# Kernel tuning notes

Measured on AMD Instinct MI355X. Metric: run time of the kernel, lower is better.

## Reference

```python
import jax, jax.numpy as jnp
import numpy as np

B = 128
IN = 256
NLVL = 6
KLVL = 3
CH = 4
C = 4 * CH * CH          # 64 channels per node
OU = 8                   # out_filter_siz_u
OV = 8                   # out_filter_siz_v
NK = 2 ** KLVL           # 8 leaf nodes per axis
W_SCALE = 1.0 / 16.0     # ~1/sqrt(2*2*C) so 7 stacked relu-convs stay numerically sane


def setup_inputs() -> dict:
    key = jax.random.key(0)
    ks = jax.random.split(key, 2 * NLVL + 4)
    fx = IN // 2 ** NLVL  # 4: input patch filter size
    inp = {}
    inp["in_data"] = jax.random.normal(ks[0], (B, IN, IN, 1), jnp.float32)
    inp["in_filter"] = jax.random.normal(ks[1], (fx, fx, 1, C), jnp.float32) * W_SCALE
    inp["in_bias"] = jnp.zeros((C,), jnp.float32)
    i = 2
    for lvl in range(1, NLVL + 1):
        n = 2 ** min(lvl, KLVL)  # node grid: grows to 2^klvl then stays
        inp[f"f{lvl}"] = jax.random.normal(ks[i], (n, n, 2, 2, C, C), jnp.float32) * W_SCALE
        inp[f"b{lvl}"] = jnp.zeros((n, n, C), jnp.float32)
        i += 1
    inp["Wd"] = jax.random.normal(ks[i], (NK, NK, 2, C, OU * OV), jnp.float32) * W_SCALE
    return inp


def _node_conv(x, w, b):
    # x: [Nu,Nv,B,H,W,C]; w: [Nu,Nv,2,2,C,C]; 2x2 stride-2 VALID conv per node
    Nu, Nv, Bn, H, W, Cc = x.shape
    xr = x.reshape(Nu, Nv, Bn, H // 2, 2, W // 2, 2, Cc)
    y = jnp.einsum('uvbhxwyc,uvxyco->uvbhwo', xr, w)
    return jax.nn.relu(y + b[:, :, None, None, None, :])


def _forward(in_data, in_filter, in_bias, fs, bs, Wd):
    Bn = in_data.shape[0]
    fx, fy = in_filter.shape[0], in_filter.shape[1]
    # input interp conv: stride == kernel -> non-overlapping patch GEMM
    xr = in_data[..., 0].reshape(Bn, in_data.shape[1] // fx, fx, in_data.shape[2] // fy, fy)
    x = jax.nn.relu(jnp.einsum('bxpyq,pqc->bxyc', xr, in_filter[:, :, 0, :]) + in_bias)
    x = x[None, None]  # [1,1,B,2^nlvl,2^nlvl,C] node grid
    for lvl in range(1, NLVL + 1):
        if lvl <= KLVL:
            # children (itu,itv) read parent (itu//2, itv//2)
            x = jnp.repeat(jnp.repeat(x, 2, axis=0), 2, axis=1)
        x = _node_conv(x, fs[lvl - 1], bs[lvl - 1])
    feats = x[:, :, :, 0, 0, :]  # [NK,NK,B,C]; spatial is 1x1 at level nlvl
    out = jnp.einsum('uvbc,uvrck->uvbrk', feats, Wd)  # r in {real, imag}
    out = out.reshape(NK, NK, Bn, 2, OU, OV)
    out = jnp.transpose(out, (2, 0, 4, 1, 5, 3))  # [B,itu,ou,itv,ov,2]
    return out.reshape(Bn, NK * OU, NK * OV, 2)


def reference(in_data, in_filter, in_bias, f1, b1, f2, b2, f3, b3, f4, b4, f5, b5, f6, b6, Wd):
    fs = (f1, f2, f3, f4, f5, f6)
    bs = (b1, b2, b3, b4, b5, b6)
    return _forward(in_data, in_filter, in_bias, fs, bs, Wd)
```

## Files before the change

### kernel.cpp

```cpp
#include <hip/hip_runtime.h>
#include <hip/hip_bf16.h>
#include <cstdint>
#include <cstddef>


typedef __attribute__((ext_vector_type(8))) short short8;
typedef __attribute__((ext_vector_type(4))) float f32x4;
typedef unsigned short ushort_t;

static __device__ __forceinline__ float b2f(const __hip_bfloat16 x) {
    return __bfloat162float(x);
}
static __device__ __forceinline__ ushort_t f2bf(float x) {
    __hip_bfloat16 h = __float2bfloat16(x);
    ushort_t u;
    __builtin_memcpy(&u, &h, 2);
    return u;
}
static __device__ __forceinline__ void gl_lds16(const void* g, void* l) {
    __builtin_amdgcn_global_load_lds(
        (const __attribute__((address_space(1))) void*)g,
        (__attribute__((address_space(3))) void*)l, 16, 0, 0);
}
#define WAIT_LGKM0() __builtin_amdgcn_s_waitcnt(0xC07F)
#define WAIT_VM0()   __builtin_amdgcn_s_waitcnt(0x0F70)

#define PREP_BLOCKS 2533

static __device__ __forceinline__ void prep_work(
    int gid, int isbf,
    const void* f1, const void* f2, const void* f3,
    const void* f4, const void* f5, const void* f6, const void* wdsrc,
    const void* b1, const void* b2, const void* b3,
    const void* b4, const void* b5, const void* b6,
    ushort_t* __restrict__ wbuf, ushort_t* __restrict__ wdbuf,
    float* __restrict__ bbuf)
{
    if (gid >= 648448) return;
    if (gid >= 630784) {
        const int bg = gid - 630784;
        const void* src; int base;
        if      (bg <   256) { src = b1; base = 0;     }
        else if (bg <  1280) { src = b2; base = 256;   }
        else if (bg <  5376) { src = b3; base = 1280;  }
        else if (bg <  9472) { src = b4; base = 5376;  }
        else if (bg < 13568) { src = b5; base = 9472;  }
        else                 { src = b6; base = 13568; }
        const int local = bg - base;
        bbuf[bg] = isbf ? b2f(((const __hip_bfloat16*)src)[local])
                        : ((const float*)src)[local];
        return;
    }
    if (gid >= 565248) {
        const int local = gid - 565248;
        const int lane = local & 63;
        const int slot = (local >> 6) & 15;
        const int site = local >> 10;
        const int ks2 = slot >> 3, nh = slot & 7, q = lane >> 4;
        const int n = nh * 16 + (lane & 15);
        const int r = n >> 6, kk = n & 63;
        const int cbase = ks2 * 32 + q * 8;
        ushort_t pk[8];
        if (isbf) {
            const ushort_t* s = (const ushort_t*)wdsrc;
            #pragma unroll
            for (int j = 0; j < 8; j++)
                pk[j] = s[(((size_t)(site * 2 + r) * 64 + cbase + j) * 64) + kk];
        } else {
            const float* s = (const float*)wdsrc;
            #pragma unroll
            for (int j = 0; j < 8; j++)
                pk[j] = f2bf(s[(((size_t)(site * 2 + r) * 64 + cbase + j) * 64) + kk]);
        }
        *(uint4*)&wdbuf[(size_t)local * 8] = *(uint4*)pk;
        return;
    }
    const void* fsrc; int base;
    if      (gid <   8192) { fsrc = f1; base = 0;      }
    else if (gid <  40960) { fsrc = f2; base = 8192;   }
    else if (gid < 172032) { fsrc = f3; base = 40960;  }
    else if (gid < 303104) { fsrc = f4; base = 172032; }
    else if (gid < 434176) { fsrc = f5; base = 303104; }
    else                   { fsrc = f6; base = 434176; }
    const int local = gid - base;
    const int lane = local & 63;
    const int slot = (local >> 6) & 7;
    const int sitetap = local >> 9;
    const int ks = slot >> 2, nh = slot & 3, q = lane >> 4;
    const int n = (lane & 15) + nh * 16;
    const int kbase = ks * 32 + q * 8;
    ushort_t pk[8];
    if (isbf) {
        const ushort_t* s = (const ushort_t*)fsrc + (size_t)sitetap * 4096;
        #pragma unroll
        for (int j = 0; j < 8; j++) pk[j] = s[(kbase + j) * 64 + n];
    } else {
        const float* s = (const float*)fsrc + (size_t)sitetap * 4096;
        #pragma unroll
        for (int j = 0; j < 8; j++) pk[j] = f2bf(s[(kbase + j) * 64 + n]);
    }
    *(uint4*)&wbuf[(size_t)gid * 8] = *(uint4*)pk;
}

static __device__ __forceinline__ void stage0_body(
    int blk, int isbf,
    const void* __restrict__ in_data, const void* __restrict__ filt,
    const void* __restrict__ bias, __hip_bfloat16* __restrict__ x0,
    int b_off, int Bc)
{
    const int X  = blk & 63;
    const int bl = blk >> 6;
    const int bg = bl + b_off;

    __shared__ float sIn[4][256];
    __shared__ float sF[16][64];
    __shared__ float sB[64];

    const int t = threadIdx.x;
    const size_t srow = ((size_t)bg * 256 + (size_t)X * 4) * 256;

    if (isbf) {
        const __hip_bfloat16* src = (const __hip_bfloat16*)in_data + srow;
        #pragma unroll
        for (int i = 0; i < 4; i++) {
            int flat = i * 256 + t;
            int p = flat >> 8, col = flat & 255;
            sIn[p][col] = b2f(src[(size_t)p * 256 + col]);
        }
        const __hip_bfloat16* fsrc = (const __hip_bfloat16*)filt;
        #pragma unroll
        for (int i = 0; i < 4; i++) {
            int flat = i * 256 + t;
            sF[flat >> 6][flat & 63] = b2f(fsrc[flat]);
        }
        if (t < 64) sB[t] = b2f(((const __hip_bfloat16*)bias)[t]);
    } else {
        const float* src = (const float*)in_data + srow;
        const int p = t >> 6, c4 = (t & 63) * 4;
        *(float4*)&sIn[p][c4] = *(const float4*)(src + (size_t)p * 256 + c4);
        const float* fsrc = (const float*)filt;
        #pragma unroll
        for (int i = 0; i < 4; i++) {
            int flat = i * 256 + t;
            sF[flat >> 6][flat & 63] = fsrc[flat];
        }
        if (t < 64) sB[t] = ((const float*)bias)[t];
    }
    __syncthreads();

    const int ty = t >> 4;
    const int tc = t & 15;

    float acc[4][4];
    {
        const float4 bv = *(const float4*)&sB[tc * 4];
        #pragma unroll
        for (int yi = 0; yi < 4; yi++) {
            acc[yi][0] = bv.x; acc[yi][1] = bv.y;
            acc[yi][2] = bv.z; acc[yi][3] = bv.w;
        }
    }

    #pragma unroll
    for (int p = 0; p < 4; p++) {
        float4 rin[4], rf[4];
        #pragma unroll
        for (int yi = 0; yi < 4; yi++)
            rin[yi] = *(const float4*)&sIn[p][ty * 16 + yi * 4];
        #pragma unroll
        for (int q = 0; q < 4; q++)
            rf[q] = *(const float4*)&sF[p * 4 + q][tc * 4];
        #pragma unroll
        for (int yi = 0; yi < 4; yi++) {
            #pragma unroll
            for (int q = 0; q < 4; q++) {
                const float a = ((const float*)&rin[yi])[q];
                acc[yi][0] = fmaf(a, rf[q].x, acc[yi][0]);
                acc[yi][1] = fmaf(a, rf[q].y, acc[yi][1]);
                acc[yi][2] = fmaf(a, rf[q].z, acc[yi][2]);
                acc[yi][3] = fmaf(a, rf[q].w, acc[yi][3]);
            }
        }
    }

    ushort_t* dst = (ushort_t*)x0;
    #pragma unroll
    for (int yi = 0; yi < 4; yi++) {
        uint2 pk;
        pk.x = (uint32_t)f2bf(fmaxf(acc[yi][0], 0.f))
             | ((uint32_t)f2bf(fmaxf(acc[yi][1], 0.f)) << 16);
        pk.y = (uint32_t)f2bf(fmaxf(acc[yi][2], 0.f))
             | ((uint32_t)f2bf(fmaxf(acc[yi][3], 0.f)) << 16);
        const int wpos = ty * 4 + yi;
        *(uint2*)(dst + ((size_t)(X * 64 + wpos) * Bc + bl) * 64 + tc * 4) = pk;
    }
}

__global__ __launch_bounds__(256) void k_prep0(
    const void* __restrict__ in_data,
    const void* f1, const void* f2, const void* f3,
    const void* f4, const void* f5, const void* f6, const void* wdsrc,
    const void* b1, const void* b2, const void* b3,
    const void* b4, const void* b5, const void* b6,
    ushort_t* __restrict__ wbuf, ushort_t* __restrict__ wdbuf,
    float* __restrict__ bbuf, int* __restrict__ flag,
    const void* __restrict__ filt, const void* __restrict__ bias0,
    __hip_bfloat16* __restrict__ x0, int Bc)
{
    __shared__ int sflag;
    const int t = threadIdx.x;
    if (t < 64) {
        const float v = __uint_as_float(((const uint32_t*)in_data)[t]);
        const bool plaus = (v == 0.0f) || (fabsf(v) > 1e-8f && fabsf(v) < 1e4f);
        const unsigned long long m = __ballot(plaus);
        if (t == 0) sflag = (__popcll(m) >= 48) ? 0 : 1;
    }
    __syncthreads();
    const int isbf = sflag;

    if (blockIdx.x < PREP_BLOCKS) {
        if (blockIdx.x == 0 && t == 0) *flag = isbf;
        prep_work(blockIdx.x * 256 + t, isbf,
                  f1, f2, f3, f4, f5, f6, wdsrc,
                  b1, b2, b3, b4, b5, b6, wbuf, wdbuf, bbuf);
    } else {
        stage0_body(blockIdx.x - PREP_BLOCKS, isbf, in_data, filt, bias0, x0, 0, Bc);
    }
}

__global__ __launch_bounds__(256) void k_stage0(
    const void* __restrict__ in_data, const void* __restrict__ filt,
    const void* __restrict__ bias, __hip_bfloat16* __restrict__ x0,
    const int* __restrict__ flag, int b_off, int Bc)
{
    stage0_body(blockIdx.x, *flag, in_data, filt, bias, x0, b_off, Bc);
}

__global__ __launch_bounds__(256, 2) void k_fused12(
    const __hip_bfloat16* __restrict__ xin,
    const ushort_t* __restrict__ w1,
    const ushort_t* __restrict__ w2,
    const float* __restrict__ b1, const float* __restrict__ b2,
    __hip_bfloat16* __restrict__ xout,
    int Bc, int mtiles)
{
    __shared__ __align__(16) ushort_t smem[27136];

    int idx = blockIdx.x;
    const int mt = idx % mtiles; idx /= mtiles;
    const int parent = idx & 3; idx >>= 2;
    const int wstrip = idx & 3;
    const int h2p = idx >> 2;
    const int ip = parent >> 1, jp = parent & 1;

    const int t = threadIdx.x;
    const int wave = t >> 6, lane = t & 63;
    const int lm = lane & 15, lq = lane >> 4;

    const size_t pstride = (size_t)Bc * 64;

    int brow = mt * 16 + lm;
    if (brow >= Bc) brow = Bc - 1;

    const ushort_t* w1site = w1 + (size_t)parent * 16384 + lane * 8;
    short8 breg[32];
    #pragma unroll
    for (int s = 0; s < 32; s++) breg[s] = *(const short8*)(w1site + s * 512);

    float bv1[4];
    #pragma unroll
    for (int fn = 0; fn < 4; fn++) bv1[fn] = b1[parent * 64 + fn * 16 + lm];

    const f32x4 zero = {0.f, 0.f, 0.f, 0.f};
    ushort_t* l1b = smem;
    const int wa = wave >> 1, wb = wave & 1;

    for (int pos = 0; pos < 4; pos++) {
        const int w2p = wstrip * 4 + pos;
        f32x4 acc[4];
        #pragma unroll
        for (int fn = 0; fn < 4; fn++) acc[fn] = zero;

        #pragma unroll
        for (int cd = 0; cd < 4; cd++) {
            const int hi0 = 4 * h2p + 2 * wa + (cd >> 1);
            const int wi0 = 4 * w2p + 2 * wb + (cd & 1);
            const __hip_bfloat16* ap =
                xin + ((size_t)hi0 * 64 + wi0) * pstride
                    + (size_t)brow * 64 + lq * 8;
            #pragma unroll
            for (int ks = 0; ks < 2; ks++) {
                short8 afr = *(const short8*)(ap + ks * 32);
                #pragma unroll
                for (int fn = 0; fn < 4; fn++)
                    acc[fn] = __builtin_amdgcn_mfma_f32_16x16x32_bf16(
                        afr, breg[cd * 8 + ks * 4 + fn], acc[fn], 0, 0, 0);
            }
        }
        ushort_t* dst = l1b + (pos * 4 + wave) * 1152;
        #pragma unroll
        for (int fn = 0; fn < 4; fn++) {
            #pragma unroll
            for (int r = 0; r < 4; r++) {
                const int m = lq * 4 + r;
                dst[m * 72 + fn * 16 + lm] =
                    f2bf(fmaxf(acc[fn][r] + bv1[fn], 0.f));
            }
        }
    }
    __syncthreads();

    {
        const int di = wave >> 1, dj = wave & 1;
        const int s2 = (2 * ip + di) * 4 + (2 * jp + dj);
        const ushort_t* w2site = w2 + (size_t)s2 * 16384 + lane * 8;
        short8 wreg[32];
        #pragma unroll
        for (int s = 0; s < 32; s++) wreg[s] = *(const short8*)(w2site + s * 512);

        float bv2[4];
        #pragma unroll
        for (int fn = 0; fn < 4; fn++) bv2[fn] = b2[s2 * 64 + fn * 16 + lm];

        ushort_t* so_buf = smem + 18432 + wave * 2176;

        for (int pos = 0; pos < 4; pos++) {
            const int w2p = wstrip * 4 + pos;
            f32x4 acc[4];
            #pragma unroll
            for (int fn = 0; fn < 4; fn++) acc[fn] = zero;

            #pragma unroll
            for (int ab = 0; ab < 4; ab++) {
                const ushort_t* sl = l1b + (pos * 4 + ab) * 1152;
                #pragma unroll
                for (int ks = 0; ks < 2; ks++) {
                    short8 afr = *(const short8*)&sl[lm * 72 + ks * 32 + lq * 8];
                    #pragma unroll
                    for (int fn = 0; fn < 4; fn++)
                        acc[fn] = __builtin_amdgcn_mfma_f32_16x16x32_bf16(
                            afr, wreg[ab * 8 + ks * 4 + fn], acc[fn], 0, 0, 0);
                }
            }

            #pragma unroll
            for (int fn = 0; fn < 4; fn++) {
                #pragma unroll
                for (int r = 0; r < 4; r++) {
                    const int m = lq * 4 + r;
                    so_buf[m * 68 + fn * 16 + lm] =
                        f2bf(fmaxf(acc[fn][r] + bv2[fn], 0.f));
                }
            }
            const size_t obase = ((size_t)s2 * 256 + h2p * 16 + w2p) * pstride;
            #pragma unroll
            for (int i2 = 0; i2 < 2; i2++) {
                const int task = i2 * 64 + lane;
                const int oct = task & 7, row = task >> 3;
                const int brw = mt * 16 + row;
                if (brw < Bc) {
                    *(uint4*)(xout + obase + (size_t)brw * 64 + oct * 8) =
                        *(const uint4*)&so_buf[row * 68 + oct * 8];
                }
            }
        }
    }
}

__global__ __launch_bounds__(256, 2) void k_level4(
    const __hip_bfloat16* __restrict__ xin,
    const ushort_t* __restrict__ wbuf,
    const float* __restrict__ bbuf,
    __hip_bfloat16* __restrict__ xout,
    int Nv_out, int HW, int Bc, int mtiles)
{
    __shared__ __align__(16) ushort_t smem[17408];

    int idx = blockIdx.x;
    const int mt = idx % mtiles; idx /= mtiles;
    const int w  = idx % HW; idx /= HW;
    const int h  = idx % HW; idx /= HW;
    const int Nv_in = Nv_out >> 1;
    const int vp = idx % Nv_in;
    const int up = idx / Nv_in;

    const int t = threadIdx.x;
    const int wave = t >> 6, lane = t & 63;
    const int lm = lane & 15, lq = lane >> 4;

    const int so = (2 * up + (wave >> 1)) * Nv_out + (2 * vp + (wave & 1));
    const int H_in = HW * 2;
    const size_t pstride = (size_t)Bc * 64;
    const size_t siteb = (size_t)(up * Nv_in + vp) * H_in * H_in * pstride;
    const ushort_t* wsite = wbuf + (size_t)so * 4 * 4096 + lane * 8;

    {
        const int hi = 2 * h + (wave >> 1), wi = 2 * w + (wave & 1);
        const size_t tapoff = siteb + ((size_t)hi * H_in + wi) * pstride;
        #pragma unroll
        for (int j = 0; j < 8; j++) {
            const int ks = j >> 2, mh = j & 3;
            int b = mt * 64 + mh * 16 + lm;
            if (b >= Bc) b = Bc - 1;
            gl_lds16(xin + tapoff + (size_t)b * 64 + ks * 32 + lq * 8,
                     &smem[(wave * 8 + j) * 512]);
        }
    }

    short8 breg[32];
    #pragma unroll
    for (int s = 0; s < 32; s++)
        breg[s] = *(const short8*)(wsite + s * 512);
    __builtin_amdgcn_sched_barrier(0);

    float bv[4];
    #pragma unroll
    for (int fn = 0; fn < 4; fn++) bv[fn] = bbuf[so * 64 + fn * 16 + lm];

    __syncthreads();

    const f32x4 zero = {0.f, 0.f, 0.f, 0.f};
    f32x4 acc[4][4];
    #pragma unroll
    for (int i = 0; i < 4; i++)
        #pragma unroll
        for (int j = 0; j < 4; j++) acc[i][j] = zero;

    #pragma unroll
    for (int tap = 0; tap < 4; tap++) {
        #pragma unroll
        for (int ks = 0; ks < 2; ks++) {
            #pragma unroll
            for (int fm = 0; fm < 4; fm++) {
                short8 a = *(const short8*)&smem[(tap * 8 + ks * 4 + fm) * 512 + lane * 8];
                #pragma unroll
                for (int fn = 0; fn < 4; fn++)
                    acc[fm][fn] = __builtin_amdgcn_mfma_f32_16x16x32_bf16(
                        a, breg[tap * 8 + ks * 4 + fn], acc[fm][fn], 0, 0, 0);
            }
        }
    }
    __syncthreads();

    ushort_t* so_buf = smem + wave * 4352;
    #pragma unroll
    for (int fm = 0; fm < 4; fm++) {
        #pragma unroll
        for (int fn = 0; fn < 4; fn++) {
            #pragma unroll
            for (int r = 0; r < 4; r++) {
                const int row = fm * 16 + lq * 4 + r;
                so_buf[row * 68 + fn * 16 + lm] =
                    f2bf(fmaxf(acc[fm][fn][r] + bv[fn], 0.f));
            }
        }
    }
    __syncthreads();

    const size_t obase = ((size_t)so * HW * HW + (size_t)h * HW + w) * pstride;
    #pragma unroll
    for (int i = 0; i < 8; i++) {
        const int task = i * 64 + lane;
        const int oct = task & 7, row = task >> 3;
        const int b = mt * 64 + row;
        if (b < Bc) {
            *(uint4*)(xout + obase + (size_t)b * 64 + oct * 8) =
                *(const uint4*)&so_buf[row * 68 + oct * 8];
        }
    }
}

__global__ __launch_bounds__(256) void k_f456(
    const __hip_bfloat16* __restrict__ xin,
    const ushort_t* __restrict__ w4, const ushort_t* __restrict__ w5,
    const ushort_t* __restrict__ w6, const ushort_t* __restrict__ wd,
    const float* __restrict__ b4, const float* __restrict__ b5,
    const float* __restrict__ b6,
    void* __restrict__ out, const int* __restrict__ flag,
    int Bc, int b_off, int mtiles)
{
    const int isbf = *flag;
    const int bx = blockIdx.x;
    const int mt = bx % mtiles;
    const int site = bx / mtiles;
    const int u = site >> 3, v = site & 7;

    __shared__ __align__(16) ushort_t smem[37376];

    const int t = threadIdx.x;
    const int wv = t >> 6, lane = t & 63;
    const int lm = lane & 15, lq = lane >> 4;

    const ushort_t* w6s = w6 + (size_t)site * 16384 + lane * 8;
    const ushort_t* wds = wd + (size_t)site * 8192  + lane * 8;

    float bv4[4], bv5[4];
    #pragma unroll
    for (int fn = 0; fn < 4; fn++) {
        bv4[fn] = b4[site * 64 + fn * 16 + lm];
        bv5[fn] = b5[site * 64 + fn * 16 + lm];
    }
    const float bv6 = b6[site * 64 + wv * 16 + lm];

    {
        const ushort_t* w4s = w4 + (size_t)site * 16384;
        #pragma unroll
        for (int s2 = 0; s2 < 8; s2++) {
            const int s = wv * 8 + s2;
            gl_lds16(w4s + s * 512 + lane * 8, &smem[s * 512]);
        }
    }
    __syncthreads();

    const f32x4 zero = {0.f, 0.f, 0.f, 0.f};
    const int h5 = wv >> 1, w5p = wv & 1;
    ushort_t* mid1w = smem + 16384 + wv * 4224;
    ushort_t* Aw = smem + 33280 + wv * 1024;
    const size_t pstride = (size_t)Bc * 64;

    int brow = mt * 16 + lm;
    if (brow >= Bc) brow = Bc - 1;
    const __hip_bfloat16* xbase =
        xin + (size_t)site * 64 * pstride + (size_t)brow * 64 + lq * 8;

    for (int i = 0; i < 4; i++) {
        const int h4 = 2 * h5 + (i >> 1), w4p = 2 * w5p + (i & 1);
        f32x4 acc[4];
        #pragma unroll
        for (int b_ = 0; b_ < 4; b_++) acc[b_] = zero;

        for (int tap = 0; tap < 4; tap++) {
            const int h3 = 2 * h4 + (tap >> 1), w3 = 2 * w4p + (tap & 1);
            const size_t poff = (size_t)(h3 * 8 + w3) * pstride;
            WAIT_LGKM0();
            #pragma unroll
            for (int ks = 0; ks < 2; ks++) {
                gl_lds16(xbase + poff + ks * 32, &Aw[ks * 512]);
            }
            WAIT_VM0();
            __builtin_amdgcn_sched_barrier(0);
            #pragma unroll
            for (int ks = 0; ks < 2; ks++) {
                short8 a = *(const short8*)&Aw[ks * 512 + lane * 8];
                #pragma unroll
                for (int fn = 0; fn < 4; fn++) {
                    short8 bfr = *(const short8*)&smem[(tap * 8 + ks * 4 + fn) * 512 + lane * 8];
                    acc[fn] = __builtin_amdgcn_mfma_f32_16x16x32_bf16(a, bfr, acc[fn], 0, 0, 0);
                }
            }
        }
        #pragma unroll
        for (int fn = 0; fn < 4; fn++) {
            #pragma unroll
            for (int r = 0; r < 4; r++) {
                const int m = lq * 4 + r;
                const int ch = fn * 16 + lm;
                mid1w[m * 264 + i * 64 + ch] =
                    f2bf(fmaxf(acc[fn][r] + bv4[fn], 0.f));
            }
        }
    }
    __syncthreads();

    {
        const ushort_t* w5s = w5 + (size_t)site * 16384;
        #pragma unroll
        for (int s2 = 0; s2 < 8; s2++) {
            const int s = wv * 8 + s2;
            gl_lds16(w5s + s * 512 + lane * 8, &smem[s * 512]);
        }
    }
    __syncthreads();

    short8 b3r[8];
    short8 wdr[4];
    {
        f32x4 acc2[4];
        #pragma unroll
        for (int b_ = 0; b_ < 4; b_++) acc2[b_] = zero;

        #pragma unroll
        for (int i = 0; i < 4; i++) {
            #pragma unroll
            for (int ks = 0; ks < 2; ks++) {
                short8 a0 = *(const short8*)&mid1w[lm * 264 + i * 64 + ks * 32 + lq * 8];
                #pragma unroll
                for (int fn = 0; fn < 4; fn++) {
                    short8 bfr = *(const short8*)&smem[(i * 8 + ks * 4 + fn) * 512 + lane * 8];
                    acc2[fn] = __builtin_amdgcn_mfma_f32_16x16x32_bf16(a0, bfr, acc2[fn], 0, 0, 0);
                }
            }
        }

        #pragma unroll
        for (int tap = 0; tap < 4; tap++)
            #pragma unroll
            for (int ks = 0; ks < 2; ks++)
                b3r[tap * 2 + ks] = *(const short8*)(w6s + (tap * 8 + ks * 4 + wv) * 512);
        #pragma unroll
        for (int ks = 0; ks < 2; ks++)
            #pragma unroll
            for (int n2 = 0; n2 < 2; n2++)
                wdr[ks * 2 + n2] = *(const short8*)(wds + (ks * 8 + 2 * wv + n2) * 512);

        #pragma unroll
        for (int fn = 0; fn < 4; fn++) {
            #pragma unroll
            for (int r = 0; r < 4; r++) {
                const int m = lq * 4 + r;
                const int ch = fn * 16 + lm;
                mid1w[m * 72 + ch] =
                    f2bf(fmaxf(acc2[fn][r] + bv5[fn], 0.f));
            }
        }
    }
    __syncthreads();

    {
        f32x4 acc3 = zero;
        #pragma unroll
        for (int tap = 0; tap < 4; tap++) {
            const ushort_t* sl = smem + 16384 + tap * 4224;
            #pragma unroll
            for (int ks = 0; ks < 2; ks++) {
                short8 a0 = *(const short8*)&sl[lm * 72 + ks * 32 + lq * 8];
                acc3 = __builtin_amdgcn_mfma_f32_16x16x32_bf16(a0, b3r[tap * 2 + ks], acc3, 0, 0, 0);
            }
        }
        ushort_t* mid3 = smem + 33280;
        #pragma unroll
        for (int r = 0; r < 4; r++) {
            const int m = lq * 4 + r;
            const int ch = wv * 16 + lm;
            mid3[m * 72 + ch] = f2bf(fmaxf(acc3[r] + bv6, 0.f));
        }
    }
    __syncthreads();

    {
        const ushort_t* mid3 = smem + 33280;
        f32x4 acc4[2];
        acc4[0] = zero; acc4[1] = zero;
        #pragma unroll
        for (int ks = 0; ks < 2; ks++) {
            short8 a0 = *(const short8*)&mid3[lm * 72 + ks * 32 + lq * 8];
            #pragma unroll
            for (int n2 = 0; n2 < 2; n2++) {
                acc4[n2] = __builtin_amdgcn_mfma_f32_16x16x32_bf16(a0, wdr[ks * 2 + n2], acc4[n2], 0, 0, 0);
            }
        }
        #pragma unroll
        for (int n2 = 0; n2 < 2; n2++) {
            const int n = (2 * wv + n2) * 16 + lm;
            const int rr = n >> 6, ou = (n >> 3) & 7, ov = n & 7;
            const size_t obase =
                (((size_t)(u * 8 + ou)) * 64 + (v * 8 + ov)) * 2 + rr;
            #pragma unroll
            for (int reg = 0; reg < 4; reg++) {
                const int brw = mt * 16 + lq * 4 + reg;
                if (brw < Bc) {
                    const size_t oidx = obase + (size_t)(b_off + brw) * 8192;
                    if (isbf) ((__hip_bfloat16*)out)[oidx] =
                        __float2bfloat16(acc4[n2][reg]);
                    else ((float*)out)[oidx] = acc4[n2][reg];
                }
            }
        }
    }
}

extern "C" void kernel_launch(void* const* d_in, const int* in_sizes, int n_in,
                              void* d_out, int out_size, void* d_ws, size_t ws_size,
                              hipStream_t stream)
{
    (void)in_sizes; (void)n_in; (void)out_size;

    const void* in_data = d_in[0];
    const void* filt    = d_in[1];
    const void* bias0   = d_in[2];
    const void* fl[7];
    const void* bl[7];
    for (int l = 1; l <= 6; l++) {
        fl[l] = d_in[1 + 2 * l];
        bl[l] = d_in[2 + 2 * l];
    }
    const void* Wd = d_in[15];

    const int Bfull = 128;
    const size_t perB = (size_t)64 * 64 * 64;

    const size_t wbufBytes  = 565248ull * 16;
    const size_t wdbufBytes = 65536ull * 16;
    const size_t bbufBytes  = 17664ull * 4;
    const size_t headBytes  = 256 + wbufBytes + wdbufBytes + bbufBytes;

    const size_t avail = ws_size > headBytes ? ws_size - headBytes : 0;
    int Bc = 0;
    for (int c = 128; c >= 1; c >>= 1) {
        if ((size_t)2 * c * perB * sizeof(__hip_bfloat16) <= avail) { Bc = c; break; }
    }
    if (Bc == 0) return;

    int* flag = (int*)d_ws;
    ushort_t* wbuf  = (ushort_t*)((char*)d_ws + 256);
    ushort_t* wdbuf = (ushort_t*)((char*)d_ws + 256 + wbufBytes);
    float* bbuf = (float*)((char*)d_ws + 256 + wbufBytes + wdbufBytes);
    __hip_bfloat16* bufA = (__hip_bfloat16*)((char*)d_ws + headBytes);
    __hip_bfloat16* bufB = bufA + (size_t)Bc * perB;

    const int mt4  = (Bc + 63) / 64;
    const int mt16 = (Bc + 15) / 16;

    for (int b_off = 0; b_off < Bfull; b_off += Bc) {
        if (b_off == 0) {
            k_prep0<<<dim3(PREP_BLOCKS + Bc * 64), 256, 0, stream>>>(
                in_data,
                fl[1], fl[2], fl[3], fl[4], fl[5], fl[6], Wd,
                bl[1], bl[2], bl[3], bl[4], bl[5], bl[6],
                wbuf, wdbuf, bbuf, flag,
                filt, bias0, bufA, Bc);
        } else {
            k_stage0<<<dim3(Bc * 64), 256, 0, stream>>>(in_data, filt, bias0, bufA, flag, b_off, Bc);
        }

        k_fused12<<<dim3(256 * mt16), 256, 0, stream>>>(
            bufA, wbuf, wbuf + 65536, bbuf, bbuf + 256, bufB, Bc, mt16);

        {
            dim3 grid(4 * 4 * 8 * 8 * mt4);
            k_level4<<<grid, 256, 0, stream>>>(bufB, wbuf + 327680,
                bbuf + 1280, bufA, 8, 8, Bc, mt4);
        }

        k_f456<<<dim3(64 * mt16), 256, 0, stream>>>(bufA,
            wbuf + 1376256, wbuf + 2424832, wbuf + 3473408, wdbuf,
            bbuf + 5376, bbuf + 9472, bbuf + 13568,
            d_out, flag, Bc, b_off, mt16);
    }
}
```

Before: 243.6 us.

## Stream weight fragments and batch four positions per MFMA loop in level kernel

Both GEMM stages of this fused level kernel stop preloading all 32 weight fragments into registers. Each weight fragment is now loaded once and applied to four spatial positions at a time, with the accumulators widened to 4x4. The A fragments for all positions are gathered up front, which gives more independent MFMAs in flight and removes the large persistent register array. The trade is more live accumulator registers and weight reloads from global memory or cache inside the inner loop.

```diff
diff --git a/kernel.cpp b/kernel.cpp
--- a/kernel.cpp
+++ b/kernel.cpp
@@ -263,9 +263,6 @@
     if (brow >= Bc) brow = Bc - 1;
 
     const ushort_t* w1site = w1 + (size_t)parent * 16384 + lane * 8;
-    short8 breg[32];
-    #pragma unroll
-    for (int s = 0; s < 32; s++) breg[s] = *(const short8*)(w1site + s * 512);
 
     float bv1[4];
     #pragma unroll
@@ -275,36 +272,48 @@
     ushort_t* l1b = smem;
     const int wa = wave >> 1, wb = wave & 1;
 
-    for (int pos = 0; pos < 4; pos++) {
-        const int w2p = wstrip * 4 + pos;
-        f32x4 acc[4];
-        #pragma unroll
-        for (int fn = 0; fn < 4; fn++) acc[fn] = zero;
+    {
+        f32x4 acc[4][4];
+        #pragma unroll
+        for (int p = 0; p < 4; p++)
+            #pragma unroll
+            for (int fn = 0; fn < 4; fn++) acc[p][fn] = zero;
 
         #pragma unroll
         for (int cd = 0; cd < 4; cd++) {
             const int hi0 = 4 * h2p + 2 * wa + (cd >> 1);
-            const int wi0 = 4 * w2p + 2 * wb + (cd & 1);
-            const __hip_bfloat16* ap =
-                xin + ((size_t)hi0 * 64 + wi0) * pstride
-                    + (size_t)brow * 64 + lq * 8;
+            const int wbase = 2 * wb + (cd & 1);
             #pragma unroll
             for (int ks = 0; ks < 2; ks++) {
-                short8 afr = *(const short8*)(ap + ks * 32);
-                #pragma unroll
-                for (int fn = 0; fn < 4; fn++)
-                    acc[fn] = __builtin_amdgcn_mfma_f32_16x16x32_bf16(
-                        afr, breg[cd * 8 + ks * 4 + fn], acc[fn], 0, 0, 0);
-            }
-        }
-        ushort_t* dst = l1b + (pos * 4 + wave) * 1152;
-        #pragma unroll
-        for (int fn = 0; fn < 4; fn++) {
-            #pragma unroll
-            for (int r = 0; r < 4; r++) {
-                const int m = lq * 4 + r;
-                dst[m * 72 + fn * 16 + lm] =
-                    f2bf(fmaxf(acc[fn][r] + bv1[fn], 0.f));
+                short8 afr[4];
+                #pragma unroll
+                for (int pos = 0; pos < 4; pos++) {
+                    const int wi0 = 4 * (wstrip * 4 + pos) + wbase;
+                    afr[pos] = *(const short8*)(
+                        xin + ((size_t)hi0 * 64 + wi0) * pstride
+                            + (size_t)brow * 64 + ks * 32 + lq * 8);
+                }
+                #pragma unroll
+                for (int fn = 0; fn < 4; fn++) {
+                    short8 bfr = *(const short8*)(w1site + (cd * 8 + ks * 4 + fn) * 512);
+                    #pragma unroll
+                    for (int pos = 0; pos < 4; pos++)
+                        acc[pos][fn] = __builtin_amdgcn_mfma_f32_16x16x32_bf16(
+                            afr[pos], bfr, acc[pos][fn], 0, 0, 0);
+                }
+            }
+        }
+        #pragma unroll
+        for (int pos = 0; pos < 4; pos++) {
+            ushort_t* dst = l1b + (pos * 4 + wave) * 1152;
+            #pragma unroll
+            for (int fn = 0; fn < 4; fn++) {
+                #pragma unroll
+                for (int r = 0; r < 4; r++) {
+                    const int m = lq * 4 + r;
+                    dst[m * 72 + fn * 16 + lm] =
+                        f2bf(fmaxf(acc[pos][fn][r] + bv1[fn], 0.f));
+                }
             }
         }
     }
@@ -314,42 +323,49 @@
         const int di = wave >> 1, dj = wave & 1;
         const int s2 = (2 * ip + di) * 4 + (2 * jp + dj);
         const ushort_t* w2site = w2 + (size_t)s2 * 16384 + lane * 8;
-        short8 wreg[32];
-        #pragma unroll
-        for (int s = 0; s < 32; s++) wreg[s] = *(const short8*)(w2site + s * 512);
 
         float bv2[4];
         #pragma unroll
         for (int fn = 0; fn < 4; fn++) bv2[fn] = b2[s2 * 64 + fn * 16 + lm];
 
+        f32x4 acc[4][4];
+        #pragma unroll
+        for (int p = 0; p < 4; p++)
+            #pragma unroll
+            for (int fn = 0; fn < 4; fn++) acc[p][fn] = zero;
+
+        #pragma unroll
+        for (int ab = 0; ab < 4; ab++) {
+            #pragma unroll
+            for (int ks = 0; ks < 2; ks++) {
+                short8 afr[4];
+                #pragma unroll
+                for (int pos = 0; pos < 4; pos++) {
+                    const ushort_t* sl = l1b + (pos * 4 + ab) * 1152;
+                    afr[pos] = *(const short8*)&sl[lm * 72 + ks * 32 + lq * 8];
+                }
+                #pragma unroll
+                for (int fn = 0; fn < 4; fn++) {
+                    short8 bfr = *(const short8*)(w2site + (ab * 8 + ks * 4 + fn) * 512);
+                    #pragma unroll
+                    for (int pos = 0; pos < 4; pos++)
+                        acc[pos][fn] = __builtin_amdgcn_mfma_f32_16x16x32_bf16(
+                            afr[pos], bfr, acc[pos][fn], 0, 0, 0);
+                }
+            }
+        }
+
         ushort_t* so_buf = smem + 18432 + wave * 2176;
-
+        #pragma unroll
         for (int pos = 0; pos < 4; pos++) {
             const int w2p = wstrip * 4 + pos;
-            f32x4 acc[4];
-            #pragma unroll
-            for (int fn = 0; fn < 4; fn++) acc[fn] = zero;
-
-            #pragma unroll
-            for (int ab = 0; ab < 4; ab++) {
-                const ushort_t* sl = l1b + (pos * 4 + ab) * 1152;
-                #pragma unroll
-                for (int ks = 0; ks < 2; ks++) {
-                    short8 afr = *(const short8*)&sl[lm * 72 + ks * 32 + lq * 8];
-                    #pragma unroll
-                    for (int fn = 0; fn < 4; fn++)
-                        acc[fn] = __builtin_amdgcn_mfma_f32_16x16x32_bf16(
-                            afr, wreg[ab * 8 + ks * 4 + fn], acc[fn], 0, 0, 0);
-                }
-            }
-
             #pragma unroll
             for (int fn = 0; fn < 4; fn++) {
                 #pragma unroll
                 for (int r = 0; r < 4; r++) {
                     const int m = lq * 4 + r;
                     so_buf[m * 68 + fn * 16 + lm] =
-                        f2bf(fmaxf(acc[fn][r] + bv2[fn], 0.f));
+                        f2bf(fmaxf(acc[pos][fn][r] + bv2[fn], 0.f));
                 }
             }
             const size_t obase = ((size_t)s2 * 256 + h2p * 16 + w2p) * pstride;
```

Result: slower. 250.1 us (+2.7%).
